# Kernel optimization log

Hardware: AMD Instinct MI355X
Metric: run time of the kernel (lower is better)

## Reference

```python
import jax, jax.numpy as jnp
import numpy as np

N_NODES = 50000
N_EDGES = 800000
IN_DIM = 256
HID = 64
HEADS = 4
OUT_DIM = 16
N_PROTO = 2
NEG_SLOPE = 0.2  # GATv2Conv default


def setup_inputs() -> dict:
    key = jax.random.key(0)
    ks = jax.random.split(key, 16)
    gat_in = HID + N_PROTO  # 66
    s = lambda k, shp: jax.random.normal(k, shp, dtype=jnp.float32) * 0.05
    return {
        "x": jax.random.normal(ks[0], (N_NODES, IN_DIM), dtype=jnp.float32),
        "edge_index": jax.random.randint(ks[1], (2, N_EDGES), 0, N_NODES, dtype=jnp.int64),
        "W_in": s(ks[2], (IN_DIM, HID)),
        "b_in": jnp.zeros((HID,), jnp.float32),
        "prototypes": s(ks[3], (N_PROTO, HID)),
        "W_l": s(ks[4], (gat_in, HEADS * HID)),
        "b_l": jnp.zeros((HEADS * HID,), jnp.float32),
        "W_r": s(ks[5], (gat_in, HEADS * HID)),
        "b_r": jnp.zeros((HEADS * HID,), jnp.float32),
        "att": s(ks[6], (HEADS, HID)),
        "gat_bias": jnp.zeros((HID,), jnp.float32),
        "W_cls": s(ks[7], (HID, OUT_DIM)),
        "b_cls": jnp.zeros((OUT_DIM,), jnp.float32),
    }


def _forward(x, edge_index, W_in, b_in, prototypes, W_l, b_l, W_r, b_r, att, gat_bias, W_cls, b_cls):
    n = x.shape[0]
    # lin_in + relu (dropout is identity in eval mode)
    h = jax.nn.relu(x @ W_in + b_in)                       # [N, HID]
    # prototype cosine similarity
    h_norm = h / (jnp.linalg.norm(h, axis=1, keepdims=True) + 1e-12)
    p_norm = prototypes / (jnp.linalg.norm(prototypes, axis=1, keepdims=True) + 1e-12)
    sem = h_norm @ p_norm.T                                # [N, 2]
    h_aug = jnp.concatenate([h, sem], axis=1)              # [N, HID+2]
    # GATv2Conv (heads=HEADS, concat=False, add_self_loops=True)
    xl = (h_aug @ W_l + b_l).reshape(n, HEADS, HID)        # source transform
    xr = (h_aug @ W_r + b_r).reshape(n, HEADS, HID)        # target transform
    loop = jnp.arange(n, dtype=edge_index.dtype)
    src = jnp.concatenate([edge_index[0], loop])           # [E+N]
    dst = jnp.concatenate([edge_index[1], loop])
    # edge-wise attention logits
    e = jax.nn.leaky_relu(xl[src] + xr[dst], NEG_SLOPE)    # [E+N, H, C]
    logits = jnp.einsum("ehc,hc->eh", e, att)              # [E+N, H]
    # segment softmax over incoming edges of each dst node
    seg_max = jax.ops.segment_max(logits, dst, num_segments=n)   # [N, H]
    alpha = jnp.exp(logits - seg_max[dst])
    denom = jax.ops.segment_sum(alpha, dst, num_segments=n)      # [N, H]
    alpha = alpha / (denom[dst] + 1e-16)
    # weighted scatter-add aggregation
    msg = xl[src] * alpha[:, :, None]                      # [E+N, H, C]
    agg = jax.ops.segment_sum(msg, dst, num_segments=n)    # [N, H, C]
    out = agg.mean(axis=1) + gat_bias                      # concat=False -> head mean
    out = jax.nn.relu(out)
    return out @ W_cls + b_cls                             # [N, OUT_DIM]


def reference(x, edge_index, W_in, b_in, prototypes, W_l, b_l, W_r, b_r, att, gat_bias, W_cls, b_cls):
    return _forward(x, edge_index, W_in, b_in, prototypes, W_l, b_l, W_r, b_r, att, gat_bias, W_cls, b_cls)
```

## Files before the change

### kernel.cpp

```cpp
#include <hip/hip_runtime.h>

#define N_NODES 50000
#define N_EDGES 800000
#define IN_DIM 256
#define HID 64
#define OUT_DIM 16
#define GAT_IN 66
#define HS_STRIDE 76
#define MEGA_BLOCKS 782
#define SCAT_BLOCKS 3125
#define CAP 64

typedef unsigned short u16;
typedef unsigned int u32;
typedef __attribute__((ext_vector_type(8))) short s8v;
typedef __attribute__((ext_vector_type(4))) float f4v;
typedef __attribute__((ext_vector_type(2))) _Float16 h2;

__device__ __forceinline__ float bf2f(u16 u) {
  union { u32 i; float f; } v; v.i = ((u32)u) << 16; return v.f;
}
__device__ __forceinline__ u16 f2bf(float f) {
  union { float f; u32 i; } v; v.f = f;
  u32 r = v.i + 0x7FFFu + ((v.i >> 16) & 1u);
  return (u16)(r >> 16);
}
__device__ __forceinline__ u16 f2h(float f) {
  union { _Float16 h; u16 u; } v; v.h = (_Float16)f; return v.u;
}
__device__ __forceinline__ void split8(const float* uu, s8v& ah, s8v& al) {
  #pragma unroll
  for (int j = 0; j < 8; ++j) {
    u32 bits = __float_as_uint(uu[j]);
    u16 hb = (u16)(bits >> 16);
    ah[j] = (short)hb;
    al[j] = (short)f2bf(uu[j] - bf2f(hb));
  }
}

__device__ __forceinline__ int probe_i64(const void* ei) {
  const long long* e64 = (const long long*)ei;
  int ok = 1;
  #pragma unroll
  for (int k = 0; k < 16; k++) {
    long long v = e64[k];
    if (v < 0 || v >= N_NODES) { ok = 0; break; }
  }
  return ok;
}

__global__ __launch_bounds__(256) void k_prep(
    const float* __restrict__ Win, const float* __restrict__ Wl,
    const float* __restrict__ Wr, const void* __restrict__ ei,
    u16* __restrict__ wbT, u16* __restrict__ wlT, u16* __restrict__ wrT,
    int* __restrict__ cnt, int* __restrict__ flags)
{
  const int gid = blockIdx.x * 256 + threadIdx.x;
  const int stride = gridDim.x * 256;
  for (int i = gid; i < N_NODES; i += stride) cnt[i] = 0;
  if (gid == 0) { flags[0] = 0; flags[1] = probe_i64(ei); }
  for (int m = gid; m < 16384; m += stride) {
    int s = m >> 11, rem = m & 2047;
    int t = rem >> 9, rem2 = rem & 511;
    int l = rem2 >> 3, j = rem2 & 7;
    int k = s * 32 + (l >> 4) * 8 + j;
    int c = t * 16 + (l & 15);
    wbT[m] = f2bf(Win[k * 64 + c]);
  }
  for (int m = gid; m < 24576; m += stride) {
    int s = m >> 13, rem = m & 8191;
    int t = rem >> 9, rem2 = rem & 511;
    int l = rem2 >> 3, j = rem2 & 7;
    int k = s * 32 + (l >> 4) * 8 + j;
    int j2 = t * 16 + (l & 15);
    u16 vl = 0, vr = 0;
    if (k < GAT_IN) {
      vl = f2bf(Wl[k * 256 + j2]);
      vr = f2bf(Wr[k * 256 + j2]);
    }
    wlT[m] = vl;
    wrT[m] = vr;
  }
}

template <int FULL>
__global__ __launch_bounds__(256) void k_work(
    const float* __restrict__ x,
    const u16* __restrict__ wbT, const float* __restrict__ bin,
    const float* __restrict__ proto,
    const u16* __restrict__ wlT, const float* __restrict__ bl,
    const u16* __restrict__ wrT, const float* __restrict__ br,
    float* __restrict__ ha, u16* __restrict__ xls, u16* __restrict__ xrs,
    const void* __restrict__ ei, const int* __restrict__ flags,
    int* __restrict__ cnt, int* __restrict__ esrc_b)
{
  if (blockIdx.x >= MEGA_BLOCKS) {
    const int e = (blockIdx.x - MEGA_BLOCKS) * 256 + threadIdx.x;
    if (e >= N_EDGES) return;
    const int isl = flags[1];
    int s, d;
    if (isl) {
      s = (int)((const long long*)ei)[e];
      d = (int)((const long long*)ei)[N_EDGES + e];
    } else {
      s = ((const int*)ei)[e];
      d = ((const int*)ei)[N_EDGES + e];
    }
    if ((unsigned)d >= N_NODES) return;
    if ((unsigned)s >= N_NODES) s = 0;
    int p = atomicAdd(&cnt[d], 1);
    if (p < CAP) esrc_b[((size_t)d << 6) + p] = s;
    return;
  }

  const int lane = threadIdx.x & 63;
  const int wv = threadIdx.x >> 6;
  const int nb = blockIdx.x * 64 + wv * 16;
  if (nb >= N_NODES) return;
  const int mrow = lane & 15, q = lane >> 4;

  __shared__ float hs_all[4][16 * HS_STRIDE];
  float* hs = hs_all[wv];

  f4v acc0 = {0.f,0.f,0.f,0.f}, acc1 = {0.f,0.f,0.f,0.f};
  f4v acc2 = {0.f,0.f,0.f,0.f}, acc3 = {0.f,0.f,0.f,0.f};
  const float* xrow = x + (size_t)(nb + mrow) * IN_DIM + q * 8;
  #pragma unroll 4
  for (int s = 0; s < 8; ++s) {
    float4 u0 = *(const float4*)(xrow + s * 32);
    float4 u1 = *(const float4*)(xrow + s * 32 + 4);
    float uu[8] = {u0.x, u0.y, u0.z, u0.w, u1.x, u1.y, u1.z, u1.w};
    s8v ah, al;
    split8(uu, ah, al);
    const u16* wp = wbT + s * 2048 + lane * 8;
    s8v b0 = *(const s8v*)(wp);
    s8v b1 = *(const s8v*)(wp + 512);
    s8v b2 = *(const s8v*)(wp + 1024);
    s8v b3 = *(const s8v*)(wp + 1536);
    acc0 = __builtin_amdgcn_mfma_f32_16x16x32_bf16(ah, b0, acc0, 0, 0, 0);
    acc0 = __builtin_amdgcn_mfma_f32_16x16x32_bf16(al, b0, acc0, 0, 0, 0);
    acc1 = __builtin_amdgcn_mfma_f32_16x16x32_bf16(ah, b1, acc1, 0, 0, 0);
    acc1 = __builtin_amdgcn_mfma_f32_16x16x32_bf16(al, b1, acc1, 0, 0, 0);
    acc2 = __builtin_amdgcn_mfma_f32_16x16x32_bf16(ah, b2, acc2, 0, 0, 0);
    acc2 = __builtin_amdgcn_mfma_f32_16x16x32_bf16(al, b2, acc2, 0, 0, 0);
    acc3 = __builtin_amdgcn_mfma_f32_16x16x32_bf16(ah, b3, acc3, 0, 0, 0);
    acc3 = __builtin_amdgcn_mfma_f32_16x16x32_bf16(al, b3, acc3, 0, 0, 0);
  }

  float bt[4], p0t[4], p1t[4];
  #pragma unroll
  for (int t = 0; t < 4; ++t) {
    bt[t]  = bin[t * 16 + mrow];
    p0t[t] = proto[t * 16 + mrow];
    p1t[t] = proto[64 + t * 16 + mrow];
  }
  float np0 = 0.f, np1 = 0.f;
  #pragma unroll
  for (int t = 0; t < 4; ++t) { np0 += p0t[t] * p0t[t]; np1 += p1t[t] * p1t[t]; }
  #pragma unroll
  for (int mm = 1; mm < 16; mm <<= 1) {
    np0 += __shfl_xor(np0, mm); np1 += __shfl_xor(np1, mm);
  }
  const float ip0 = 1.f / (sqrtf(np0) + 1e-12f);
  const float ip1 = 1.f / (sqrtf(np1) + 1e-12f);

  float hcol[4][4];
  #pragma unroll
  for (int r = 0; r < 4; ++r) {
    hcol[0][r] = fmaxf(acc0[r] + bt[0], 0.f);
    hcol[1][r] = fmaxf(acc1[r] + bt[1], 0.f);
    hcol[2][r] = fmaxf(acc2[r] + bt[2], 0.f);
    hcol[3][r] = fmaxf(acc3[r] + bt[3], 0.f);
  }
  #pragma unroll
  for (int r = 0; r < 4; ++r) {
    float r0 = 0.f, r1 = 0.f, r2 = 0.f;
    #pragma unroll
    for (int t = 0; t < 4; ++t) {
      float h = hcol[t][r];
      r0 += h * h; r1 += h * p0t[t]; r2 += h * p1t[t];
    }
    #pragma unroll
    for (int mm = 1; mm < 16; mm <<= 1) {
      r0 += __shfl_xor(r0, mm); r1 += __shfl_xor(r1, mm); r2 += __shfl_xor(r2, mm);
    }
    const int node = q * 4 + r;
    #pragma unroll
    for (int t = 0; t < 4; ++t)
      hs[node * HS_STRIDE + t * 16 + mrow] = hcol[t][r];
    if (!FULL) {
      float* row = ha + (size_t)(nb + node) * 68;
      #pragma unroll
      for (int t = 0; t < 4; ++t) row[t * 16 + mrow] = hcol[t][r];
    }
    if (mrow == 0) {
      float hi = 1.f / (sqrtf(r0) + 1e-12f);
      float s0 = r1 * hi * ip0, s1 = r2 * hi * ip1;
      hs[node * HS_STRIDE + 64] = s0;
      hs[node * HS_STRIDE + 65] = s1;
      if (!FULL) {
        float* row = ha + (size_t)(nb + node) * 68;
        row[64] = s0; row[65] = s1;
      }
    }
  }

  s8v ahs[3], als[3];
  #pragma unroll
  for (int s = 0; s < 3; ++s) {
    float uu[8];
    if (s < 2) {
      float4 u0 = *(const float4*)(hs + mrow * HS_STRIDE + s * 32 + q * 8);
      float4 u1 = *(const float4*)(hs + mrow * HS_STRIDE + s * 32 + q * 8 + 4);
      uu[0]=u0.x; uu[1]=u0.y; uu[2]=u0.z; uu[3]=u0.w;
      uu[4]=u1.x; uu[5]=u1.y; uu[6]=u1.z; uu[7]=u1.w;
    } else {
      #pragma unroll
      for (int j = 0; j < 8; ++j) uu[j] = 0.f;
      if (q == 0) {
        uu[0] = hs[mrow * HS_STRIDE + 64];
        uu[1] = hs[mrow * HS_STRIDE + 65];
      }
    }
    split8(uu, ahs[s], als[s]);
  }

  #pragma unroll 2
  for (int t = 0; t < 16; ++t) {
    f4v accl = {0.f, 0.f, 0.f, 0.f};
    f4v accr = {0.f, 0.f, 0.f, 0.f};
    #pragma unroll
    for (int s = 0; s < 3; ++s) {
      s8v bvl = *(const s8v*)(wlT + s * 8192 + t * 512 + lane * 8);
      accl = __builtin_amdgcn_mfma_f32_16x16x32_bf16(ahs[s], bvl, accl, 0, 0, 0);
      accl = __builtin_amdgcn_mfma_f32_16x16x32_bf16(als[s], bvl, accl, 0, 0, 0);
    }
    if (FULL) {
      #pragma unroll
      for (int s = 0; s < 3; ++s) {
        s8v bvr = *(const s8v*)(wrT + s * 8192 + t * 512 + lane * 8);
        accr = __builtin_amdgcn_mfma_f32_16x16x32_bf16(ahs[s], bvr, accr, 0, 0, 0);
        accr = __builtin_amdgcn_mfma_f32_16x16x32_bf16(als[s], bvr, accr, 0, 0, 0);
      }
    }
    float bcl = bl[t * 16 + mrow];
    #pragma unroll
    for (int r = 0; r < 4; ++r)
      xls[(size_t)(nb + q * 4 + r) * 256 + t * 16 + mrow] = f2h(accl[r] + bcl);
    if (FULL) {
      float bcr = br[t * 16 + mrow];
      #pragma unroll
      for (int r = 0; r < 4; ++r)
        xrs[(size_t)(nb + q * 4 + r) * 256 + t * 16 + mrow] = f2h(accr[r] + bcr);
    }
  }
}

template <int CTRL>
__device__ __forceinline__ float dppadd(float g) {
  return g + __int_as_float(__builtin_amdgcn_update_dpp(
      0, __float_as_int(g), CTRL, 0xF, 0xF, true));
}

__device__ __forceinline__ float red16_dpp(float g) {
  g = dppadd<0xB1>(g);
  g = dppadd<0x4E>(g);
  g = dppadd<0x124>(g);
  g = dppadd<0x128>(g);
  return g;
}

__device__ __forceinline__ float edge_h(uint2 rv, h2 xr01, h2 xr23,
                                        h2 av01, h2 av23,
                                        h2& x01, h2& x23) {
  x01 = __builtin_bit_cast(h2, rv.x);
  x23 = __builtin_bit_cast(h2, rv.y);
  h2 t01 = x01 + xr01, t23 = x23 + xr23;
  t01 = __builtin_elementwise_max(t01, t01 * (_Float16)0.2f);
  t23 = __builtin_elementwise_max(t23, t23 * (_Float16)0.2f);
  float g = __builtin_amdgcn_fdot2(t01, av01, 0.f, false);
  return __builtin_amdgcn_fdot2(t23, av23, g, false);
}

template <int INLINE_XR>
__global__ __launch_bounds__(256) void k_agg(
    const u16* __restrict__ xls, const u16* __restrict__ xrs,
    const float* __restrict__ ha, const float* __restrict__ Wr,
    const float* __restrict__ br,
    const int* __restrict__ esrc_b, const int* __restrict__ cnt,
    const float* __restrict__ att, const float* __restrict__ gbias,
    const float* __restrict__ wcls, const float* __restrict__ bcls,
    float* __restrict__ out)
{
  __shared__ u16 wr[INLINE_XR ? GAT_IN * 256 : 64];
  if (INLINE_XR) {
    for (int m = threadIdx.x; m < GAT_IN * 256; m += 256) wr[m] = f2bf(Wr[m]);
    __syncthreads();
  }
  const int lane = threadIdx.x & 63;
  const int n = __builtin_amdgcn_readfirstlane(blockIdx.x * 4 + (threadIdx.x >> 6));
  if (n >= N_NODES) return;

  float4 avr = *(const float4*)(att + lane * 4);
  const h2 av01 = {(_Float16)avr.x, (_Float16)avr.y};
  const h2 av23 = {(_Float16)avr.z, (_Float16)avr.w};

  h2 xr01, xr23;
  if (INLINE_XR) {
    float4 bv = *(const float4*)(br + lane * 4);
    float y0 = bv.x, y1 = bv.y, y2 = bv.z, y3 = bv.w;
    const float* hrow = ha + (size_t)n * 68;
    for (int i = 0; i < GAT_IN; ++i) {
      ushort4 wv = *(const ushort4*)&wr[i * 256 + lane * 4];
      float hv = hrow[i];
      y0 += hv * bf2f(wv.x); y1 += hv * bf2f(wv.y);
      y2 += hv * bf2f(wv.z); y3 += hv * bf2f(wv.w);
    }
    xr01 = (h2){(_Float16)y0, (_Float16)y1};
    xr23 = (h2){(_Float16)y2, (_Float16)y3};
  } else {
    uint2 qv = *(const uint2*)(xrs + (size_t)n * 256 + lane * 4);
    xr01 = __builtin_bit_cast(h2, qv.x);
    xr23 = __builtin_bit_cast(h2, qv.y);
  }

  const int kb = n << 6;
  int dg = __builtin_amdgcn_readfirstlane(cnt[n]);
  if (dg < 0) dg = 0;
  if (dg > CAP) dg = CAP;
  const int ke = kb + dg;
  const int nq = dg >> 2;

  const char* __restrict__ xb = (const char*)xls;
  const u32 loff = (u32)lane * 8u;
  #define GROW(s) (*(const uint2*)(xb + ((((u32)(s)) << 9) + loff)))

  uint2 p0, p1, p2, p3;
  uint2 n0, n1, n2, n3;
  int j0 = 0, j1 = 0, j2 = 0, j3 = 0;
  if (nq > 0) {
    int a0 = esrc_b[kb], a1 = esrc_b[kb + 1], a2 = esrc_b[kb + 2], a3 = esrc_b[kb + 3];
    p0 = GROW(a0); p1 = GROW(a1); p2 = GROW(a2); p3 = GROW(a3);
    if (nq > 1) {
      int b0 = esrc_b[kb + 4], b1 = esrc_b[kb + 5], b2 = esrc_b[kb + 6], b3 = esrc_b[kb + 7];
      n0 = GROW(b0); n1 = GROW(b1); n2 = GROW(b2); n3 = GROW(b3);
      if (nq > 2) {
        j0 = esrc_b[kb + 8];  j1 = esrc_b[kb + 9];
        j2 = esrc_b[kb + 10]; j3 = esrc_b[kb + 11];
      }
    }
  }

  float l_, c0, c1, c2, c3;
  {
    uint2 rv = GROW(n);
    h2 x01, x23;
    float g = edge_h(rv, xr01, xr23, av01, av23, x01, x23);
    g = red16_dpp(g);
    float a = __expf(fminf(g, 60.f));
    l_ = a;
    c0 = a * (float)x01[0]; c1 = a * (float)x01[1];
    c2 = a * (float)x23[0]; c3 = a * (float)x23[1];
  }

  for (int q = 0; q < nq; ++q) {
    uint2 r0 = p0, r1 = p1, r2 = p2, r3 = p3;
    p0 = n0; p1 = n1; p2 = n2; p3 = n3;
    if (q + 2 < nq) {
      n0 = GROW(j0); n1 = GROW(j1); n2 = GROW(j2); n3 = GROW(j3);
      if (q + 3 < nq) {
        int ib = kb + (q + 3) * 4;
        j0 = esrc_b[ib];     j1 = esrc_b[ib + 1];
        j2 = esrc_b[ib + 2]; j3 = esrc_b[ib + 3];
      }
    }
    h2 xa01, xa23, xb01, xb23, xc01, xc23, xd01, xd23;
    float g0 = edge_h(r0, xr01, xr23, av01, av23, xa01, xa23);
    float g1 = edge_h(r1, xr01, xr23, av01, av23, xb01, xb23);
    float g2 = edge_h(r2, xr01, xr23, av01, av23, xc01, xc23);
    float g3 = edge_h(r3, xr01, xr23, av01, av23, xd01, xd23);
    g0 = red16_dpp(g0); g1 = red16_dpp(g1);
    g2 = red16_dpp(g2); g3 = red16_dpp(g3);
    float a0 = __expf(fminf(g0, 60.f));
    float a1 = __expf(fminf(g1, 60.f));
    float a2 = __expf(fminf(g2, 60.f));
    float a3 = __expf(fminf(g3, 60.f));
    l_ += (a0 + a1) + (a2 + a3);
    c0 += a0 * (float)xa01[0] + a1 * (float)xb01[0]
        + a2 * (float)xc01[0] + a3 * (float)xd01[0];
    c1 += a0 * (float)xa01[1] + a1 * (float)xb01[1]
        + a2 * (float)xc01[1] + a3 * (float)xd01[1];
    c2 += a0 * (float)xa23[0] + a1 * (float)xb23[0]
        + a2 * (float)xc23[0] + a3 * (float)xd23[0];
    c3 += a0 * (float)xa23[1] + a1 * (float)xb23[1]
        + a2 * (float)xc23[1] + a3 * (float)xd23[1];
  }

  for (int i = kb + nq * 4; i < ke; ++i) {
    int s = esrc_b[i];
    uint2 rv = GROW(s);
    h2 x01, x23;
    float g = edge_h(rv, xr01, xr23, av01, av23, x01, x23);
    g = red16_dpp(g);
    float a = __expf(fminf(g, 60.f));
    l_ += a;
    c0 += a * (float)x01[0]; c1 += a * (float)x01[1];
    c2 += a * (float)x23[0]; c3 += a * (float)x23[1];
  }
  #undef GROW

  float inv = 1.f / (l_ + 1e-16f);
  float v0 = c0 * inv, v1 = c1 * inv, v2 = c2 * inv, v3 = c3 * inv;
  v0 += __shfl_xor(v0, 16); v0 += __shfl_xor(v0, 32);
  v1 += __shfl_xor(v1, 16); v1 += __shfl_xor(v1, 32);
  v2 += __shfl_xor(v2, 16); v2 += __shfl_xor(v2, 32);
  v3 += __shfl_xor(v3, 16); v3 += __shfl_xor(v3, 32);
  const int g4 = (lane & 15) * 4;
  const int h = lane >> 4;
  float4 gb = *(const float4*)(gbias + g4);
  v0 = fmaxf(0.25f * v0 + gb.x, 0.f);
  v1 = fmaxf(0.25f * v1 + gb.y, 0.f);
  v2 = fmaxf(0.25f * v2 + gb.z, 0.f);
  v3 = fmaxf(0.25f * v3 + gb.w, 0.f);
  float4 w0 = *(const float4*)(wcls + (g4 + 0) * 16 + h * 4);
  float4 w1 = *(const float4*)(wcls + (g4 + 1) * 16 + h * 4);
  float4 w2 = *(const float4*)(wcls + (g4 + 2) * 16 + h * 4);
  float4 w3 = *(const float4*)(wcls + (g4 + 3) * 16 + h * 4);
  float o0 = v0 * w0.x + v1 * w1.x + v2 * w2.x + v3 * w3.x;
  float o1 = v0 * w0.y + v1 * w1.y + v2 * w2.y + v3 * w3.y;
  float o2 = v0 * w0.z + v1 * w1.z + v2 * w2.z + v3 * w3.z;
  float o3 = v0 * w0.w + v1 * w1.w + v2 * w2.w + v3 * w3.w;
  #pragma unroll
  for (int mm = 1; mm < 16; mm <<= 1) {
    o0 += __shfl_xor(o0, mm); o1 += __shfl_xor(o1, mm);
    o2 += __shfl_xor(o2, mm); o3 += __shfl_xor(o3, mm);
  }
  if ((lane & 15) == 0) {
    float4 bcv = *(const float4*)(bcls + h * 4);
    float4 ov;
    ov.x = o0 + bcv.x; ov.y = o1 + bcv.y; ov.z = o2 + bcv.z; ov.w = o3 + bcv.w;
    *(float4*)(out + (size_t)n * 16 + h * 4) = ov;
  }
}

extern "C" void kernel_launch(void* const* d_in, const int* in_sizes, int n_in,
                              void* d_out, int out_size, void* d_ws, size_t ws_size,
                              hipStream_t stream)
{
  const float* x     = (const float*)d_in[0];
  const void*  ei    = d_in[1];
  const float* Win   = (const float*)d_in[2];
  const float* bin   = (const float*)d_in[3];
  const float* proto = (const float*)d_in[4];
  const float* Wl    = (const float*)d_in[5];
  const float* bl    = (const float*)d_in[6];
  const float* Wr    = (const float*)d_in[7];
  const float* br    = (const float*)d_in[8];
  const float* att   = (const float*)d_in[9];
  const float* gbias = (const float*)d_in[10];
  const float* wcls  = (const float*)d_in[11];
  const float* bcls  = (const float*)d_in[12];
  float* out = (float*)d_out;

  char* p = (char*)d_ws;
  size_t used = 0;
  auto carve = [&](size_t bytes) {
    char* q = p + used;
    used += (bytes + 255) & ~(size_t)255;
    return (void*)q;
  };
  int* flags  = (int*)carve(256);
  int* cnt    = (int*)carve(N_NODES * 4);
  int* esrc_b = (int*)carve((size_t)N_NODES * CAP * 4);
  u16* wbT    = (u16*)carve(16384 * 2);
  u16* wlT    = (u16*)carve(24576 * 2);
  u16* wrT    = (u16*)carve(24576 * 2);
  u16* xls    = (u16*)carve((size_t)N_NODES * 256 * 2);
  const size_t base = used;
  void* big = carve((size_t)N_NODES * 256 * 2);
  float* ha = (float*)big;
  u16* xrs  = (u16*)big;
  const bool full = ws_size >= base + (size_t)N_NODES * 256 * 2;

  k_prep<<<196, 256, 0, stream>>>(Win, Wl, Wr, ei, wbT, wlT, wrT, cnt, flags);
  if (full)
    k_work<1><<<MEGA_BLOCKS + SCAT_BLOCKS, 256, 0, stream>>>(
        x, wbT, bin, proto, wlT, bl, wrT, br, ha, xls, xrs,
        ei, flags, cnt, esrc_b);
  else
    k_work<0><<<MEGA_BLOCKS + SCAT_BLOCKS, 256, 0, stream>>>(
        x, wbT, bin, proto, wlT, bl, wrT, br, ha, xls, xrs,
        ei, flags, cnt, esrc_b);
  if (full)
    k_agg<0><<<12500, 256, 0, stream>>>(xls, xrs, ha, Wr, br, esrc_b, cnt,
                                        att, gbias, wcls, bcls, out);
  else
    k_agg<1><<<12500, 256, 0, stream>>>(xls, xrs, ha, Wr, br, esrc_b, cnt,
                                        att, gbias, wcls, bcls, out);
}
```

Measured before the change: 236.3 us.

## Merge prep, transform/scatter and aggregation into one cooperative persistent kernel

Replaces the three separate launches (weight prep, node transform plus edge scatter, aggregation) with one cooperative kernel that uses grid-wide syncs between phases. Blocks are split so about four fifths run the node-transform MFMA work while the rest do the edge bucketing concurrently, and the aggregation then loops persistently over nodes. The aim is to remove launch gaps and kernel tail effects. In exchange it adds grid.sync costs, caps the grid at occupancy times CU count, and introduces static host-side caching of device properties.

```diff
diff --git a/kernel.cpp b/kernel.cpp
--- a/kernel.cpp
+++ b/kernel.cpp
@@ -1,4 +1,7 @@
 #include <hip/hip_runtime.h>
+#include <hip/hip_cooperative_groups.h>
+
+namespace cg = cooperative_groups;
 
 #define N_NODES 50000
 #define N_EDGES 800000
@@ -7,8 +10,8 @@
 #define OUT_DIM 16
 #define GAT_IN 66
 #define HS_STRIDE 76
-#define MEGA_BLOCKS 782
-#define SCAT_BLOCKS 3125
+#define MEGA_ITERS 782
+#define AGG_ITERS 12500
 #define CAP 64
 
 typedef unsigned short u16;
@@ -37,7 +40,6 @@
     al[j] = (short)f2bf(uu[j] - bf2f(hb));
   }
 }
-
 __device__ __forceinline__ int probe_i64(const void* ei) {
   const long long* e64 = (const long long*)ei;
   int ok = 1;
@@ -49,219 +51,11 @@
   return ok;
 }
 
-__global__ __launch_bounds__(256) void k_prep(
-    const float* __restrict__ Win, const float* __restrict__ Wl,
-    const float* __restrict__ Wr, const void* __restrict__ ei,
-    u16* __restrict__ wbT, u16* __restrict__ wlT, u16* __restrict__ wrT,
-    int* __restrict__ cnt, int* __restrict__ flags)
-{
-  const int gid = blockIdx.x * 256 + threadIdx.x;
-  const int stride = gridDim.x * 256;
-  for (int i = gid; i < N_NODES; i += stride) cnt[i] = 0;
-  if (gid == 0) { flags[0] = 0; flags[1] = probe_i64(ei); }
-  for (int m = gid; m < 16384; m += stride) {
-    int s = m >> 11, rem = m & 2047;
-    int t = rem >> 9, rem2 = rem & 511;
-    int l = rem2 >> 3, j = rem2 & 7;
-    int k = s * 32 + (l >> 4) * 8 + j;
-    int c = t * 16 + (l & 15);
-    wbT[m] = f2bf(Win[k * 64 + c]);
-  }
-  for (int m = gid; m < 24576; m += stride) {
-    int s = m >> 13, rem = m & 8191;
-    int t = rem >> 9, rem2 = rem & 511;
-    int l = rem2 >> 3, j = rem2 & 7;
-    int k = s * 32 + (l >> 4) * 8 + j;
-    int j2 = t * 16 + (l & 15);
-    u16 vl = 0, vr = 0;
-    if (k < GAT_IN) {
-      vl = f2bf(Wl[k * 256 + j2]);
-      vr = f2bf(Wr[k * 256 + j2]);
-    }
-    wlT[m] = vl;
-    wrT[m] = vr;
-  }
-}
-
-template <int FULL>
-__global__ __launch_bounds__(256) void k_work(
-    const float* __restrict__ x,
-    const u16* __restrict__ wbT, const float* __restrict__ bin,
-    const float* __restrict__ proto,
-    const u16* __restrict__ wlT, const float* __restrict__ bl,
-    const u16* __restrict__ wrT, const float* __restrict__ br,
-    float* __restrict__ ha, u16* __restrict__ xls, u16* __restrict__ xrs,
-    const void* __restrict__ ei, const int* __restrict__ flags,
-    int* __restrict__ cnt, int* __restrict__ esrc_b)
-{
-  if (blockIdx.x >= MEGA_BLOCKS) {
-    const int e = (blockIdx.x - MEGA_BLOCKS) * 256 + threadIdx.x;
-    if (e >= N_EDGES) return;
-    const int isl = flags[1];
-    int s, d;
-    if (isl) {
-      s = (int)((const long long*)ei)[e];
-      d = (int)((const long long*)ei)[N_EDGES + e];
-    } else {
-      s = ((const int*)ei)[e];
-      d = ((const int*)ei)[N_EDGES + e];
-    }
-    if ((unsigned)d >= N_NODES) return;
-    if ((unsigned)s >= N_NODES) s = 0;
-    int p = atomicAdd(&cnt[d], 1);
-    if (p < CAP) esrc_b[((size_t)d << 6) + p] = s;
-    return;
-  }
-
-  const int lane = threadIdx.x & 63;
-  const int wv = threadIdx.x >> 6;
-  const int nb = blockIdx.x * 64 + wv * 16;
-  if (nb >= N_NODES) return;
-  const int mrow = lane & 15, q = lane >> 4;
-
-  __shared__ float hs_all[4][16 * HS_STRIDE];
-  float* hs = hs_all[wv];
-
-  f4v acc0 = {0.f,0.f,0.f,0.f}, acc1 = {0.f,0.f,0.f,0.f};
-  f4v acc2 = {0.f,0.f,0.f,0.f}, acc3 = {0.f,0.f,0.f,0.f};
-  const float* xrow = x + (size_t)(nb + mrow) * IN_DIM + q * 8;
-  #pragma unroll 4
-  for (int s = 0; s < 8; ++s) {
-    float4 u0 = *(const float4*)(xrow + s * 32);
-    float4 u1 = *(const float4*)(xrow + s * 32 + 4);
-    float uu[8] = {u0.x, u0.y, u0.z, u0.w, u1.x, u1.y, u1.z, u1.w};
-    s8v ah, al;
-    split8(uu, ah, al);
-    const u16* wp = wbT + s * 2048 + lane * 8;
-    s8v b0 = *(const s8v*)(wp);
-    s8v b1 = *(const s8v*)(wp + 512);
-    s8v b2 = *(const s8v*)(wp + 1024);
-    s8v b3 = *(const s8v*)(wp + 1536);
-    acc0 = __builtin_amdgcn_mfma_f32_16x16x32_bf16(ah, b0, acc0, 0, 0, 0);
-    acc0 = __builtin_amdgcn_mfma_f32_16x16x32_bf16(al, b0, acc0, 0, 0, 0);
-    acc1 = __builtin_amdgcn_mfma_f32_16x16x32_bf16(ah, b1, acc1, 0, 0, 0);
-    acc1 = __builtin_amdgcn_mfma_f32_16x16x32_bf16(al, b1, acc1, 0, 0, 0);
-    acc2 = __builtin_amdgcn_mfma_f32_16x16x32_bf16(ah, b2, acc2, 0, 0, 0);
-    acc2 = __builtin_amdgcn_mfma_f32_16x16x32_bf16(al, b2, acc2, 0, 0, 0);
-    acc3 = __builtin_amdgcn_mfma_f32_16x16x32_bf16(ah, b3, acc3, 0, 0, 0);
-    acc3 = __builtin_amdgcn_mfma_f32_16x16x32_bf16(al, b3, acc3, 0, 0, 0);
-  }
-
-  float bt[4], p0t[4], p1t[4];
-  #pragma unroll
-  for (int t = 0; t < 4; ++t) {
-    bt[t]  = bin[t * 16 + mrow];
-    p0t[t] = proto[t * 16 + mrow];
-    p1t[t] = proto[64 + t * 16 + mrow];
-  }
-  float np0 = 0.f, np1 = 0.f;
-  #pragma unroll
-  for (int t = 0; t < 4; ++t) { np0 += p0t[t] * p0t[t]; np1 += p1t[t] * p1t[t]; }
-  #pragma unroll
-  for (int mm = 1; mm < 16; mm <<= 1) {
-    np0 += __shfl_xor(np0, mm); np1 += __shfl_xor(np1, mm);
-  }
-  const float ip0 = 1.f / (sqrtf(np0) + 1e-12f);
-  const float ip1 = 1.f / (sqrtf(np1) + 1e-12f);
-
-  float hcol[4][4];
-  #pragma unroll
-  for (int r = 0; r < 4; ++r) {
-    hcol[0][r] = fmaxf(acc0[r] + bt[0], 0.f);
-    hcol[1][r] = fmaxf(acc1[r] + bt[1], 0.f);
-    hcol[2][r] = fmaxf(acc2[r] + bt[2], 0.f);
-    hcol[3][r] = fmaxf(acc3[r] + bt[3], 0.f);
-  }
-  #pragma unroll
-  for (int r = 0; r < 4; ++r) {
-    float r0 = 0.f, r1 = 0.f, r2 = 0.f;
-    #pragma unroll
-    for (int t = 0; t < 4; ++t) {
-      float h = hcol[t][r];
-      r0 += h * h; r1 += h * p0t[t]; r2 += h * p1t[t];
-    }
-    #pragma unroll
-    for (int mm = 1; mm < 16; mm <<= 1) {
-      r0 += __shfl_xor(r0, mm); r1 += __shfl_xor(r1, mm); r2 += __shfl_xor(r2, mm);
-    }
-    const int node = q * 4 + r;
-    #pragma unroll
-    for (int t = 0; t < 4; ++t)
-      hs[node * HS_STRIDE + t * 16 + mrow] = hcol[t][r];
-    if (!FULL) {
-      float* row = ha + (size_t)(nb + node) * 68;
-      #pragma unroll
-      for (int t = 0; t < 4; ++t) row[t * 16 + mrow] = hcol[t][r];
-    }
-    if (mrow == 0) {
-      float hi = 1.f / (sqrtf(r0) + 1e-12f);
-      float s0 = r1 * hi * ip0, s1 = r2 * hi * ip1;
-      hs[node * HS_STRIDE + 64] = s0;
-      hs[node * HS_STRIDE + 65] = s1;
-      if (!FULL) {
-        float* row = ha + (size_t)(nb + node) * 68;
-        row[64] = s0; row[65] = s1;
-      }
-    }
-  }
-
-  s8v ahs[3], als[3];
-  #pragma unroll
-  for (int s = 0; s < 3; ++s) {
-    float uu[8];
-    if (s < 2) {
-      float4 u0 = *(const float4*)(hs + mrow * HS_STRIDE + s * 32 + q * 8);
-      float4 u1 = *(const float4*)(hs + mrow * HS_STRIDE + s * 32 + q * 8 + 4);
-      uu[0]=u0.x; uu[1]=u0.y; uu[2]=u0.z; uu[3]=u0.w;
-      uu[4]=u1.x; uu[5]=u1.y; uu[6]=u1.z; uu[7]=u1.w;
-    } else {
-      #pragma unroll
-      for (int j = 0; j < 8; ++j) uu[j] = 0.f;
-      if (q == 0) {
-        uu[0] = hs[mrow * HS_STRIDE + 64];
-        uu[1] = hs[mrow * HS_STRIDE + 65];
-      }
-    }
-    split8(uu, ahs[s], als[s]);
-  }
-
-  #pragma unroll 2
-  for (int t = 0; t < 16; ++t) {
-    f4v accl = {0.f, 0.f, 0.f, 0.f};
-    f4v accr = {0.f, 0.f, 0.f, 0.f};
-    #pragma unroll
-    for (int s = 0; s < 3; ++s) {
-      s8v bvl = *(const s8v*)(wlT + s * 8192 + t * 512 + lane * 8);
-      accl = __builtin_amdgcn_mfma_f32_16x16x32_bf16(ahs[s], bvl, accl, 0, 0, 0);
-      accl = __builtin_amdgcn_mfma_f32_16x16x32_bf16(als[s], bvl, accl, 0, 0, 0);
-    }
-    if (FULL) {
-      #pragma unroll
-      for (int s = 0; s < 3; ++s) {
-        s8v bvr = *(const s8v*)(wrT + s * 8192 + t * 512 + lane * 8);
-        accr = __builtin_amdgcn_mfma_f32_16x16x32_bf16(ahs[s], bvr, accr, 0, 0, 0);
-        accr = __builtin_amdgcn_mfma_f32_16x16x32_bf16(als[s], bvr, accr, 0, 0, 0);
-      }
-    }
-    float bcl = bl[t * 16 + mrow];
-    #pragma unroll
-    for (int r = 0; r < 4; ++r)
-      xls[(size_t)(nb + q * 4 + r) * 256 + t * 16 + mrow] = f2h(accl[r] + bcl);
-    if (FULL) {
-      float bcr = br[t * 16 + mrow];
-      #pragma unroll
-      for (int r = 0; r < 4; ++r)
-        xrs[(size_t)(nb + q * 4 + r) * 256 + t * 16 + mrow] = f2h(accr[r] + bcr);
-    }
-  }
-}
-
 template <int CTRL>
 __device__ __forceinline__ float dppadd(float g) {
   return g + __int_as_float(__builtin_amdgcn_update_dpp(
       0, __float_as_int(g), CTRL, 0xF, 0xF, true));
 }
-
 __device__ __forceinline__ float red16_dpp(float g) {
   g = dppadd<0xB1>(g);
   g = dppadd<0x4E>(g);
@@ -269,7 +63,6 @@
   g = dppadd<0x128>(g);
   return g;
 }
-
 __device__ __forceinline__ float edge_h(uint2 rv, h2 xr01, h2 xr23,
                                         h2 av01, h2 av23,
                                         h2& x01, h2& x23) {
@@ -282,165 +75,378 @@
   return __builtin_amdgcn_fdot2(t23, av23, g, false);
 }
 
-template <int INLINE_XR>
-__global__ __launch_bounds__(256) void k_agg(
-    const u16* __restrict__ xls, const u16* __restrict__ xrs,
-    const float* __restrict__ ha, const float* __restrict__ Wr,
-    const float* __restrict__ br,
-    const int* __restrict__ esrc_b, const int* __restrict__ cnt,
+template <int FULL>
+__global__ __launch_bounds__(256) void k_all(
+    const float* __restrict__ x, const void* __restrict__ ei,
+    const float* __restrict__ Win, const float* __restrict__ bin,
+    const float* __restrict__ proto,
+    const float* __restrict__ Wl, const float* __restrict__ bl,
+    const float* __restrict__ Wr, const float* __restrict__ br,
     const float* __restrict__ att, const float* __restrict__ gbias,
     const float* __restrict__ wcls, const float* __restrict__ bcls,
+    u16* __restrict__ wbT, u16* __restrict__ wlT, u16* __restrict__ wrT,
+    int* __restrict__ cnt, int* __restrict__ flags, int* __restrict__ esrc_b,
+    float* __restrict__ ha, u16* __restrict__ xls, u16* __restrict__ xrs,
     float* __restrict__ out)
 {
-  __shared__ u16 wr[INLINE_XR ? GAT_IN * 256 : 64];
-  if (INLINE_XR) {
+  cg::grid_group grid = cg::this_grid();
+  const int G = gridDim.x;
+  const int gid = blockIdx.x * 256 + threadIdx.x;
+  const int gstride = G * 256;
+  const int lane = threadIdx.x & 63;
+  const int wv = threadIdx.x >> 6;
+
+  constexpr int HS_BYTES = 4 * 16 * HS_STRIDE * 4;
+  constexpr int WR_BYTES = GAT_IN * 256 * 2;
+  constexpr int SMEM = FULL ? HS_BYTES : (WR_BYTES > HS_BYTES ? WR_BYTES : HS_BYTES);
+  __shared__ __align__(16) char smem[SMEM];
+
+  for (int i = gid; i < N_NODES; i += gstride) cnt[i] = 0;
+  if (gid == 0) flags[1] = probe_i64(ei);
+  for (int m = gid; m < 16384; m += gstride) {
+    int s = m >> 11, rem = m & 2047;
+    int t = rem >> 9, rem2 = rem & 511;
+    int l = rem2 >> 3, j = rem2 & 7;
+    int k = s * 32 + (l >> 4) * 8 + j;
+    int c = t * 16 + (l & 15);
+    wbT[m] = f2bf(Win[k * 64 + c]);
+  }
+  for (int m = gid; m < 24576; m += gstride) {
+    int s = m >> 13, rem = m & 8191;
+    int t = rem >> 9, rem2 = rem & 511;
+    int l = rem2 >> 3, j = rem2 & 7;
+    int k = s * 32 + (l >> 4) * 8 + j;
+    int j2 = t * 16 + (l & 15);
+    u16 vl = 0, vr = 0;
+    if (k < GAT_IN) {
+      vl = f2bf(Wl[k * 256 + j2]);
+      vr = f2bf(Wr[k * 256 + j2]);
+    }
+    wlT[m] = vl;
+    wrT[m] = vr;
+  }
+  grid.sync();
+
+  int Gm = (G * 4) / 5;
+  if (Gm > MEGA_ITERS) Gm = MEGA_ITERS;
+  if (Gm < 1) Gm = 1;
+  if (Gm >= G) Gm = G - 1;
+
+  if (blockIdx.x < Gm) {
+    float* hs = (float*)smem + wv * (16 * HS_STRIDE);
+    for (int b = blockIdx.x; b < MEGA_ITERS; b += Gm) {
+      const int nb = b * 64 + wv * 16;
+      if (nb < N_NODES) {
+        const int mrow = lane & 15, q = lane >> 4;
+        f4v acc0 = {0.f,0.f,0.f,0.f}, acc1 = {0.f,0.f,0.f,0.f};
+        f4v acc2 = {0.f,0.f,0.f,0.f}, acc3 = {0.f,0.f,0.f,0.f};
+        const float* xrow = x + (size_t)(nb + mrow) * IN_DIM + q * 8;
+        #pragma unroll 4
+        for (int s = 0; s < 8; ++s) {
+          float4 u0 = *(const float4*)(xrow + s * 32);
+          float4 u1 = *(const float4*)(xrow + s * 32 + 4);
+          float uu[8] = {u0.x, u0.y, u0.z, u0.w, u1.x, u1.y, u1.z, u1.w};
+          s8v ah, al;
+          split8(uu, ah, al);
+          const u16* wp = wbT + s * 2048 + lane * 8;
+          s8v b0 = *(const s8v*)(wp);
+          s8v b1 = *(const s8v*)(wp + 512);
+          s8v b2 = *(const s8v*)(wp + 1024);
+          s8v b3 = *(const s8v*)(wp + 1536);
+          acc0 = __builtin_amdgcn_mfma_f32_16x16x32_bf16(ah, b0, acc0, 0, 0, 0);
+          acc0 = __builtin_amdgcn_mfma_f32_16x16x32_bf16(al, b0, acc0, 0, 0, 0);
+          acc1 = __builtin_amdgcn_mfma_f32_16x16x32_bf16(ah, b1, acc1, 0, 0, 0);
+          acc1 = __builtin_amdgcn_mfma_f32_16x16x32_bf16(al, b1, acc1, 0, 0, 0);
+          acc2 = __builtin_amdgcn_mfma_f32_16x16x32_bf16(ah, b2, acc2, 0, 0, 0);
+          acc2 = __builtin_amdgcn_mfma_f32_16x16x32_bf16(al, b2, acc2, 0, 0, 0);
+          acc3 = __builtin_amdgcn_mfma_f32_16x16x32_bf16(ah, b3, acc3, 0, 0, 0);
+          acc3 = __builtin_amdgcn_mfma_f32_16x16x32_bf16(al, b3, acc3, 0, 0, 0);
+        }
+
+        float bt[4], p0t[4], p1t[4];
+        #pragma unroll
+        for (int t = 0; t < 4; ++t) {
+          bt[t]  = bin[t * 16 + mrow];
+          p0t[t] = proto[t * 16 + mrow];
+          p1t[t] = proto[64 + t * 16 + mrow];
+        }
+        float np0 = 0.f, np1 = 0.f;
+        #pragma unroll
+        for (int t = 0; t < 4; ++t) { np0 += p0t[t] * p0t[t]; np1 += p1t[t] * p1t[t]; }
+        #pragma unroll
+        for (int mm = 1; mm < 16; mm <<= 1) {
+          np0 += __shfl_xor(np0, mm); np1 += __shfl_xor(np1, mm);
+        }
+        const float ip0 = 1.f / (sqrtf(np0) + 1e-12f);
+        const float ip1 = 1.f / (sqrtf(np1) + 1e-12f);
+
+        float hcol[4][4];
+        #pragma unroll
+        for (int r = 0; r < 4; ++r) {
+          hcol[0][r] = fmaxf(acc0[r] + bt[0], 0.f);
+          hcol[1][r] = fmaxf(acc1[r] + bt[1], 0.f);
+          hcol[2][r] = fmaxf(acc2[r] + bt[2], 0.f);
+          hcol[3][r] = fmaxf(acc3[r] + bt[3], 0.f);
+        }
+        #pragma unroll
+        for (int r = 0; r < 4; ++r) {
+          float r0 = 0.f, r1 = 0.f, r2 = 0.f;
+          #pragma unroll
+          for (int t = 0; t < 4; ++t) {
+            float h = hcol[t][r];
+            r0 += h * h; r1 += h * p0t[t]; r2 += h * p1t[t];
+          }
+          #pragma unroll
+          for (int mm = 1; mm < 16; mm <<= 1) {
+            r0 += __shfl_xor(r0, mm); r1 += __shfl_xor(r1, mm); r2 += __shfl_xor(r2, mm);
+          }
+          const int node = q * 4 + r;
+          #pragma unroll
+          for (int t = 0; t < 4; ++t)
+            hs[node * HS_STRIDE + t * 16 + mrow] = hcol[t][r];
+          if (!FULL) {
+            float* row = ha + (size_t)(nb + node) * 68;
+            #pragma unroll
+            for (int t = 0; t < 4; ++t) row[t * 16 + mrow] = hcol[t][r];
+          }
+          if (mrow == 0) {
+            float hi = 1.f / (sqrtf(r0) + 1e-12f);
+            float s0 = r1 * hi * ip0, s1 = r2 * hi * ip1;
+            hs[node * HS_STRIDE + 64] = s0;
+            hs[node * HS_STRIDE + 65] = s1;
+            if (!FULL) {
+              float* row = ha + (size_t)(nb + node) * 68;
+              row[64] = s0; row[65] = s1;
+            }
+          }
+        }
+
+        s8v ahs[3], als[3];
+        #pragma unroll
+        for (int s = 0; s < 3; ++s) {
+          float uu[8];
+          if (s < 2) {
+            float4 u0 = *(const float4*)(hs + mrow * HS_STRIDE + s * 32 + q * 8);
+            float4 u1 = *(const float4*)(hs + mrow * HS_STRIDE + s * 32 + q * 8 + 4);
+            uu[0]=u0.x; uu[1]=u0.y; uu[2]=u0.z; uu[3]=u0.w;
+            uu[4]=u1.x; uu[5]=u1.y; uu[6]=u1.z; uu[7]=u1.w;
+          } else {
+            #pragma unroll
+            for (int j = 0; j < 8; ++j) uu[j] = 0.f;
+            if (q == 0) {
+              uu[0] = hs[mrow * HS_STRIDE + 64];
+              uu[1] = hs[mrow * HS_STRIDE + 65];
+            }
+          }
+          split8(uu, ahs[s], als[s]);
+        }
+
+        #pragma unroll 2
+        for (int t = 0; t < 16; ++t) {
+          f4v accl = {0.f, 0.f, 0.f, 0.f};
+          f4v accr = {0.f, 0.f, 0.f, 0.f};
+          #pragma unroll
+          for (int s = 0; s < 3; ++s) {
+            s8v bvl = *(const s8v*)(wlT + s * 8192 + t * 512 + lane * 8);
+            accl = __builtin_amdgcn_mfma_f32_16x16x32_bf16(ahs[s], bvl, accl, 0, 0, 0);
+            accl = __builtin_amdgcn_mfma_f32_16x16x32_bf16(als[s], bvl, accl, 0, 0, 0);
+          }
+          if (FULL) {
+            #pragma unroll
+            for (int s = 0; s < 3; ++s) {
+              s8v bvr = *(const s8v*)(wrT + s * 8192 + t * 512 + lane * 8);
+              accr = __builtin_amdgcn_mfma_f32_16x16x32_bf16(ahs[s], bvr, accr, 0, 0, 0);
+              accr = __builtin_amdgcn_mfma_f32_16x16x32_bf16(als[s], bvr, accr, 0, 0, 0);
+            }
+          }
+          float bcl = bl[t * 16 + mrow];
+          #pragma unroll
+          for (int r = 0; r < 4; ++r)
+            xls[(size_t)(nb + q * 4 + r) * 256 + t * 16 + mrow] = f2h(accl[r] + bcl);
+          if (FULL) {
+            float bcr = br[t * 16 + mrow];
+            #pragma unroll
+            for (int r = 0; r < 4; ++r)
+              xrs[(size_t)(nb + q * 4 + r) * 256 + t * 16 + mrow] = f2h(accr[r] + bcr);
+          }
+        }
+      }
+    }
+  } else {
+    const int isl = flags[1];
+    const int t0 = (blockIdx.x - Gm) * 256 + threadIdx.x;
+    const int sstr = (G - Gm) * 256;
+    if (isl) {
+      const long long* es = (const long long*)ei;
+      for (int e = t0; e < N_EDGES; e += sstr) {
+        int s = (int)es[e], d = (int)es[N_EDGES + e];
+        if ((unsigned)d >= N_NODES) continue;
+        if ((unsigned)s >= N_NODES) s = 0;
+        int p = atomicAdd(&cnt[d], 1);
+        if (p < CAP) esrc_b[((size_t)d << 6) + p] = s;
+      }
+    } else {
+      const int* es = (const int*)ei;
+      for (int e = t0; e < N_EDGES; e += sstr) {
+        int s = es[e], d = es[N_EDGES + e];
+        if ((unsigned)d >= N_NODES) continue;
+        if ((unsigned)s >= N_NODES) s = 0;
+        int p = atomicAdd(&cnt[d], 1);
+        if (p < CAP) esrc_b[((size_t)d << 6) + p] = s;
+      }
+    }
+  }
+  grid.sync();
+
+  u16* wr = (u16*)smem;
+  if (!FULL) {
     for (int m = threadIdx.x; m < GAT_IN * 256; m += 256) wr[m] = f2bf(Wr[m]);
     __syncthreads();
   }
-  const int lane = threadIdx.x & 63;
-  const int n = __builtin_amdgcn_readfirstlane(blockIdx.x * 4 + (threadIdx.x >> 6));
-  if (n >= N_NODES) return;
-
   float4 avr = *(const float4*)(att + lane * 4);
   const h2 av01 = {(_Float16)avr.x, (_Float16)avr.y};
   const h2 av23 = {(_Float16)avr.z, (_Float16)avr.w};
-
-  h2 xr01, xr23;
-  if (INLINE_XR) {
-    float4 bv = *(const float4*)(br + lane * 4);
-    float y0 = bv.x, y1 = bv.y, y2 = bv.z, y3 = bv.w;
-    const float* hrow = ha + (size_t)n * 68;
-    for (int i = 0; i < GAT_IN; ++i) {
-      ushort4 wv = *(const ushort4*)&wr[i * 256 + lane * 4];
-      float hv = hrow[i];
-      y0 += hv * bf2f(wv.x); y1 += hv * bf2f(wv.y);
-      y2 += hv * bf2f(wv.z); y3 += hv * bf2f(wv.w);
-    }
-    xr01 = (h2){(_Float16)y0, (_Float16)y1};
-    xr23 = (h2){(_Float16)y2, (_Float16)y3};
-  } else {
-    uint2 qv = *(const uint2*)(xrs + (size_t)n * 256 + lane * 4);
-    xr01 = __builtin_bit_cast(h2, qv.x);
-    xr23 = __builtin_bit_cast(h2, qv.y);
-  }
-
-  const int kb = n << 6;
-  int dg = __builtin_amdgcn_readfirstlane(cnt[n]);
-  if (dg < 0) dg = 0;
-  if (dg > CAP) dg = CAP;
-  const int ke = kb + dg;
-  const int nq = dg >> 2;
-
-  const char* __restrict__ xb = (const char*)xls;
+  const char* __restrict__ xbp = (const char*)xls;
   const u32 loff = (u32)lane * 8u;
-  #define GROW(s) (*(const uint2*)(xb + ((((u32)(s)) << 9) + loff)))
-
-  uint2 p0, p1, p2, p3;
-  uint2 n0, n1, n2, n3;
-  int j0 = 0, j1 = 0, j2 = 0, j3 = 0;
-  if (nq > 0) {
-    int a0 = esrc_b[kb], a1 = esrc_b[kb + 1], a2 = esrc_b[kb + 2], a3 = esrc_b[kb + 3];
-    p0 = GROW(a0); p1 = GROW(a1); p2 = GROW(a2); p3 = GROW(a3);
-    if (nq > 1) {
-      int b0 = esrc_b[kb + 4], b1 = esrc_b[kb + 5], b2 = esrc_b[kb + 6], b3 = esrc_b[kb + 7];
-      n0 = GROW(b0); n1 = GROW(b1); n2 = GROW(b2); n3 = GROW(b3);
-      if (nq > 2) {
-        j0 = esrc_b[kb + 8];  j1 = esrc_b[kb + 9];
-        j2 = esrc_b[kb + 10]; j3 = esrc_b[kb + 11];
+  #define GROW(s) (*(const uint2*)(xbp + ((((u32)(s)) << 9) + loff)))
+
+  for (int blk = blockIdx.x; blk < AGG_ITERS; blk += G) {
+    const int n = __builtin_amdgcn_readfirstlane(blk * 4 + wv);
+    if (n >= N_NODES) continue;
+
+    h2 xr01, xr23;
+    if (!FULL) {
+      float4 bv = *(const float4*)(br + lane * 4);
+      float y0 = bv.x, y1 = bv.y, y2 = bv.z, y3 = bv.w;
+      const float* hrow = ha + (size_t)n * 68;
+      for (int i = 0; i < GAT_IN; ++i) {
+        ushort4 wvv = *(const ushort4*)&wr[i * 256 + lane * 4];
+        float hv = hrow[i];
+        y0 += hv * bf2f(wvv.x); y1 += hv * bf2f(wvv.y);
+        y2 += hv * bf2f(wvv.z); y3 += hv * bf2f(wvv.w);
       }
-    }
-  }
-
-  float l_, c0, c1, c2, c3;
-  {
-    uint2 rv = GROW(n);
-    h2 x01, x23;
-    float g = edge_h(rv, xr01, xr23, av01, av23, x01, x23);
-    g = red16_dpp(g);
-    float a = __expf(fminf(g, 60.f));
-    l_ = a;
-    c0 = a * (float)x01[0]; c1 = a * (float)x01[1];
-    c2 = a * (float)x23[0]; c3 = a * (float)x23[1];
-  }
-
-  for (int q = 0; q < nq; ++q) {
-    uint2 r0 = p0, r1 = p1, r2 = p2, r3 = p3;
-    p0 = n0; p1 = n1; p2 = n2; p3 = n3;
-    if (q + 2 < nq) {
-      n0 = GROW(j0); n1 = GROW(j1); n2 = GROW(j2); n3 = GROW(j3);
-      if (q + 3 < nq) {
-        int ib = kb + (q + 3) * 4;
-        j0 = esrc_b[ib];     j1 = esrc_b[ib + 1];
-        j2 = esrc_b[ib + 2]; j3 = esrc_b[ib + 3];
+      xr01 = (h2){(_Float16)y0, (_Float16)y1};
+      xr23 = (h2){(_Float16)y2, (_Float16)y3};
+    } else {
+      uint2 qv = *(const uint2*)(xrs + (size_t)n * 256 + lane * 4);
+      xr01 = __builtin_bit_cast(h2, qv.x);
+      xr23 = __builtin_bit_cast(h2, qv.y);
+    }
+
+    const int kb = n << 6;
+    int dg = __builtin_amdgcn_readfirstlane(cnt[n]);
+    if (dg < 0) dg = 0;
+    if (dg > CAP) dg = CAP;
+    const int ke = kb + dg;
+    const int nq = dg >> 2;
+
+    uint2 p0, p1, p2, p3;
+    uint2 n0, n1, n2, n3;
+    int j0 = 0, j1 = 0, j2 = 0, j3 = 0;
+    if (nq > 0) {
+      int a0 = esrc_b[kb], a1 = esrc_b[kb + 1], a2 = esrc_b[kb + 2], a3 = esrc_b[kb + 3];
+      p0 = GROW(a0); p1 = GROW(a1); p2 = GROW(a2); p3 = GROW(a3);
+      if (nq > 1) {
+        int b0 = esrc_b[kb + 4], b1 = esrc_b[kb + 5], b2 = esrc_b[kb + 6], b3 = esrc_b[kb + 7];
+        n0 = GROW(b0); n1 = GROW(b1); n2 = GROW(b2); n3 = GROW(b3);
+        if (nq > 2) {
+          j0 = esrc_b[kb + 8];  j1 = esrc_b[kb + 9];
+          j2 = esrc_b[kb + 10]; j3 = esrc_b[kb + 11];
+        }
       }
     }
-    h2 xa01, xa23, xb01, xb23, xc01, xc23, xd01, xd23;
-    float g0 = edge_h(r0, xr01, xr23, av01, av23, xa01, xa23);
-    float g1 = edge_h(r1, xr01, xr23, av01, av23, xb01, xb23);
-    float g2 = edge_h(r2, xr01, xr23, av01, av23, xc01, xc23);
-    float g3 = edge_h(r3, xr01, xr23, av01, av23, xd01, xd23);
-    g0 = red16_dpp(g0); g1 = red16_dpp(g1);
-    g2 = red16_dpp(g2); g3 = red16_dpp(g3);
-    float a0 = __expf(fminf(g0, 60.f));
-    float a1 = __expf(fminf(g1, 60.f));
-    float a2 = __expf(fminf(g2, 60.f));
-    float a3 = __expf(fminf(g3, 60.f));
-    l_ += (a0 + a1) + (a2 + a3);
-    c0 += a0 * (float)xa01[0] + a1 * (float)xb01[0]
-        + a2 * (float)xc01[0] + a3 * (float)xd01[0];
-    c1 += a0 * (float)xa01[1] + a1 * (float)xb01[1]
-        + a2 * (float)xc01[1] + a3 * (float)xd01[1];
-    c2 += a0 * (float)xa23[0] + a1 * (float)xb23[0]
-        + a2 * (float)xc23[0] + a3 * (float)xd23[0];
-    c3 += a0 * (float)xa23[1] + a1 * (float)xb23[1]
-        + a2 * (float)xc23[1] + a3 * (float)xd23[1];
-  }
-
-  for (int i = kb + nq * 4; i < ke; ++i) {
-    int s = esrc_b[i];
-    uint2 rv = GROW(s);
-    h2 x01, x23;
-    float g = edge_h(rv, xr01, xr23, av01, av23, x01, x23);
-    g = red16_dpp(g);
-    float a = __expf(fminf(g, 60.f));
-    l_ += a;
-    c0 += a * (float)x01[0]; c1 += a * (float)x01[1];
-    c2 += a * (float)x23[0]; c3 += a * (float)x23[1];
+
+    float l_, c0, c1, c2, c3;
+    {
+      uint2 rv = GROW(n);
+      h2 x01, x23;
+      float g = edge_h(rv, xr01, xr23, av01, av23, x01, x23);
+      g = red16_dpp(g);
+      float a = __expf(fminf(g, 60.f));
+      l_ = a;
+      c0 = a * (float)x01[0]; c1 = a * (float)x01[1];
+      c2 = a * (float)x23[0]; c3 = a * (float)x23[1];
+    }
+
+    for (int q = 0; q < nq; ++q) {
+      uint2 r0 = p0, r1 = p1, r2 = p2, r3 = p3;
+      p0 = n0; p1 = n1; p2 = n2; p3 = n3;
+      if (q + 2 < nq) {
+        n0 = GROW(j0); n1 = GROW(j1); n2 = GROW(j2); n3 = GROW(j3);
+        if (q + 3 < nq) {
+          int ib = kb + (q + 3) * 4;
+          j0 = esrc_b[ib];     j1 = esrc_b[ib + 1];
+          j2 = esrc_b[ib + 2]; j3 = esrc_b[ib + 3];
+        }
+      }
+      h2 xa01, xa23, xb01, xb23, xc01, xc23, xd01, xd23;
+      float g0 = edge_h(r0, xr01, xr23, av01, av23, xa01, xa23);
+      float g1 = edge_h(r1, xr01, xr23, av01, av23, xb01, xb23);
+      float g2 = edge_h(r2, xr01, xr23, av01, av23, xc01, xc23);
+      float g3 = edge_h(r3, xr01, xr23, av01, av23, xd01, xd23);
+      g0 = red16_dpp(g0); g1 = red16_dpp(g1);
+      g2 = red16_dpp(g2); g3 = red16_dpp(g3);
+      float a0 = __expf(fminf(g0, 60.f));
+      float a1 = __expf(fminf(g1, 60.f));
+      float a2 = __expf(fminf(g2, 60.f));
+      float a3 = __expf(fminf(g3, 60.f));
+      l_ += (a0 + a1) + (a2 + a3);
+      c0 += a0 * (float)xa01[0] + a1 * (float)xb01[0]
+          + a2 * (float)xc01[0] + a3 * (float)xd01[0];
+      c1 += a0 * (float)xa01[1] + a1 * (float)xb01[1]
+          + a2 * (float)xc01[1] + a3 * (float)xd01[1];
+      c2 += a0 * (float)xa23[0] + a1 * (float)xb23[0]
+          + a2 * (float)xc23[0] + a3 * (float)xd23[0];
+      c3 += a0 * (float)xa23[1] + a1 * (float)xb23[1]
+          + a2 * (float)xc23[1] + a3 * (float)xd23[1];
+    }
+
+    for (int i = kb + nq * 4; i < ke; ++i) {
+      int s = esrc_b[i];
+      uint2 rv = GROW(s);
+      h2 x01, x23;
+      float g = edge_h(rv, xr01, xr23, av01, av23, x01, x23);
+      g = red16_dpp(g);
+      float a = __expf(fminf(g, 60.f));
+      l_ += a;
+      c0 += a * (float)x01[0]; c1 += a * (float)x01[1];
+      c2 += a * (float)x23[0]; c3 += a * (float)x23[1];
+    }
+
+    float inv = 1.f / (l_ + 1e-16f);
+    float v0 = c0 * inv, v1 = c1 * inv, v2 = c2 * inv, v3 = c3 * inv;
+    v0 += __shfl_xor(v0, 16); v0 += __shfl_xor(v0, 32);
+    v1 += __shfl_xor(v1, 16); v1 += __shfl_xor(v1, 32);
+    v2 += __shfl_xor(v2, 16); v2 += __shfl_xor(v2, 32);
+    v3 += __shfl_xor(v3, 16); v3 += __shfl_xor(v3, 32);
+    const int g4 = (lane & 15) * 4;
+    const int h = lane >> 4;
+    float4 gb = *(const float4*)(gbias + g4);
+    v0 = fmaxf(0.25f * v0 + gb.x, 0.f);
+    v1 = fmaxf(0.25f * v1 + gb.y, 0.f);
+    v2 = fmaxf(0.25f * v2 + gb.z, 0.f);
+    v3 = fmaxf(0.25f * v3 + gb.w, 0.f);
+    float4 w0 = *(const float4*)(wcls + (g4 + 0) * 16 + h * 4);
+    float4 w1 = *(const float4*)(wcls + (g4 + 1) * 16 + h * 4);
+    float4 w2 = *(const float4*)(wcls + (g4 + 2) * 16 + h * 4);
+    float4 w3 = *(const float4*)(wcls + (g4 + 3) * 16 + h * 4);
+    float o0 = v0 * w0.x + v1 * w1.x + v2 * w2.x + v3 * w3.x;
+    float o1 = v0 * w0.y + v1 * w1.y + v2 * w2.y + v3 * w3.y;
+    float o2 = v0 * w0.z + v1 * w1.z + v2 * w2.z + v3 * w3.z;
+    float o3 = v0 * w0.w + v1 * w1.w + v2 * w2.w + v3 * w3.w;
+    #pragma unroll
+    for (int mm = 1; mm < 16; mm <<= 1) {
+      o0 += __shfl_xor(o0, mm); o1 += __shfl_xor(o1, mm);
+      o2 += __shfl_xor(o2, mm); o3 += __shfl_xor(o3, mm);
+    }
+    if ((lane & 15) == 0) {
+      float4 bcv = *(const float4*)(bcls + h * 4);
+      float4 ov;
+      ov.x = o0 + bcv.x; ov.y = o1 + bcv.y; ov.z = o2 + bcv.z; ov.w = o3 + bcv.w;
+      *(float4*)(out + (size_t)n * 16 + h * 4) = ov;
+    }
   }
   #undef GROW
-
-  float inv = 1.f / (l_ + 1e-16f);
-  float v0 = c0 * inv, v1 = c1 * inv, v2 = c2 * inv, v3 = c3 * inv;
-  v0 += __shfl_xor(v0, 16); v0 += __shfl_xor(v0, 32);
-  v1 += __shfl_xor(v1, 16); v1 += __shfl_xor(v1, 32);
-  v2 += __shfl_xor(v2, 16); v2 += __shfl_xor(v2, 32);
-  v3 += __shfl_xor(v3, 16); v3 += __shfl_xor(v3, 32);
-  const int g4 = (lane & 15) * 4;
-  const int h = lane >> 4;
-  float4 gb = *(const float4*)(gbias + g4);
-  v0 = fmaxf(0.25f * v0 + gb.x, 0.f);
-  v1 = fmaxf(0.25f * v1 + gb.y, 0.f);
-  v2 = fmaxf(0.25f * v2 + gb.z, 0.f);
-  v3 = fmaxf(0.25f * v3 + gb.w, 0.f);
-  float4 w0 = *(const float4*)(wcls + (g4 + 0) * 16 + h * 4);
-  float4 w1 = *(const float4*)(wcls + (g4 + 1) * 16 + h * 4);
-  float4 w2 = *(const float4*)(wcls + (g4 + 2) * 16 + h * 4);
-  float4 w3 = *(const float4*)(wcls + (g4 + 3) * 16 + h * 4);
-  float o0 = v0 * w0.x + v1 * w1.x + v2 * w2.x + v3 * w3.x;
-  float o1 = v0 * w0.y + v1 * w1.y + v2 * w2.y + v3 * w3.y;
-  float o2 = v0 * w0.z + v1 * w1.z + v2 * w2.z + v3 * w3.z;
-  float o3 = v0 * w0.w + v1 * w1.w + v2 * w2.w + v3 * w3.w;
-  #pragma unroll
-  for (int mm = 1; mm < 16; mm <<= 1) {
-    o0 += __shfl_xor(o0, mm); o1 += __shfl_xor(o1, mm);
-    o2 += __shfl_xor(o2, mm); o3 += __shfl_xor(o3, mm);
-  }
-  if ((lane & 15) == 0) {
-    float4 bcv = *(const float4*)(bcls + h * 4);
-    float4 ov;
-    ov.x = o0 + bcv.x; ov.y = o1 + bcv.y; ov.z = o2 + bcv.z; ov.w = o3 + bcv.w;
-    *(float4*)(out + (size_t)n * 16 + h * 4) = ov;
-  }
 }
 
 extern "C" void kernel_launch(void* const* d_in, const int* in_sizes, int n_in,
@@ -482,19 +488,49 @@
   u16* xrs  = (u16*)big;
   const bool full = ws_size >= base + (size_t)N_NODES * 256 * 2;
 
-  k_prep<<<196, 256, 0, stream>>>(Win, Wl, Wr, ei, wbT, wlT, wrT, cnt, flags);
-  if (full)
-    k_work<1><<<MEGA_BLOCKS + SCAT_BLOCKS, 256, 0, stream>>>(
-        x, wbT, bin, proto, wlT, bl, wrT, br, ha, xls, xrs,
-        ei, flags, cnt, esrc_b);
-  else
-    k_work<0><<<MEGA_BLOCKS + SCAT_BLOCKS, 256, 0, stream>>>(
-        x, wbT, bin, proto, wlT, bl, wrT, br, ha, xls, xrs,
-        ei, flags, cnt, esrc_b);
-  if (full)
-    k_agg<0><<<12500, 256, 0, stream>>>(xls, xrs, ha, Wr, br, esrc_b, cnt,
-                                        att, gbias, wcls, bcls, out);
-  else
-    k_agg<1><<<12500, 256, 0, stream>>>(xls, xrs, ha, Wr, br, esrc_b, cnt,
-                                        att, gbias, wcls, bcls, out);
-}
+  static int grid_full = 0, grid_fb = 0, num_cu = 0;
+  if (num_cu == 0) {
+    hipDeviceProp_t prop;
+    int dev = 0;
+    if (hipGetDevice(&dev) != hipSuccess) dev = 0;
+    if (hipGetDeviceProperties(&prop, dev) == hipSuccess)
+      num_cu = prop.multiProcessorCount;
+    else
+      num_cu = 256;
+  }
+  void* args[] = {
+    (void*)&x, (void*)&ei, (void*)&Win, (void*)&bin, (void*)&proto,
+    (void*)&Wl, (void*)&bl, (void*)&Wr, (void*)&br,
+    (void*)&att, (void*)&gbias, (void*)&wcls, (void*)&bcls,
+    (void*)&wbT, (void*)&wlT, (void*)&wrT,
+    (void*)&cnt, (void*)&flags, (void*)&esrc_b,
+    (void*)&ha, (void*)&xls, (void*)&xrs, (void*)&out
+  };
+  if (full) {
+    if (grid_full == 0) {
+      int mb = 0;
+      if (hipOccupancyMaxActiveBlocksPerMultiprocessor(&mb, k_all<1>, 256, 0)
+              != hipSuccess || mb < 1)
+        mb = 4;
+      long g = (long)mb * num_cu;
+      if (g > 2048) g = 2048;
+      if (g < 2) g = 2;
+      grid_full = (int)g;
+    }
+    hipLaunchCooperativeKernel(k_all<1>, dim3(grid_full), dim3(256),
+                               args, 0, stream);
+  } else {
+    if (grid_fb == 0) {
+      int mb = 0;
+      if (hipOccupancyMaxActiveBlocksPerMultiprocessor(&mb, k_all<0>, 256, 0)
+              != hipSuccess || mb < 1)
+        mb = 2;
+      long g = (long)mb * num_cu;
+      if (g > 2048) g = 2048;
+      if (g < 2) g = 2;
+      grid_fb = (int)g;
+    }
+    hipLaunchCooperativeKernel(k_all<0>, dim3(grid_fb), dim3(256),
+                               args, 0, stream);
+  }
+}
```

After: 462.8 us. +95.9%, slower.
